# Optimization experiments

Hardware: AMD Instinct MI355X
Metric: run time of the kernel (lower is better)

## Reference

```python
import jax, jax.numpy as jnp
import numpy as np


def _gelu(x):
    # torch nn.GELU default is the exact erf form
    return jax.nn.gelu(x, approximate=False)


def setup_inputs() -> dict:
    key = jax.random.key(0)
    B, C, H, W = 4, 64, 256, 256   # batch, width, grid
    L, M1, M2 = 2, 32, 32          # retained blocks, Fourier modes per corner
    HM, P, O = 128, 256, 1         # channel-MLP hidden, projection hidden, out channels
    ks = jax.random.split(key, 16)
    n = lambda k, s, sc=1.0: jax.random.normal(k, s, dtype=jnp.float32) * sc
    spec = 1.0 / (C * C)           # classic FNO spectral-weight init scale
    fan = 1.0 / np.sqrt(C).astype(np.float32)
    return {
        "x": n(ks[0], (B, C, H, W)),
        # spectral weights: last dim 2 = (real, imag); sw1 -> low-freq corner, sw2 -> high-freq corner
        "sw1": n(ks[1], (L, C, C, M1, M2, 2), spec),
        "sw2": n(ks[2], (L, C, C, M1, M2, 2), spec),
        "skip_w": n(ks[3], (L, C, C), fan),
        "skip_b": n(ks[4], (L, C), 0.01),
        "mlp_w1": n(ks[5], (L, HM, C), fan),
        "mlp_b1": n(ks[6], (L, HM), 0.01),
        "mlp_w2": n(ks[7], (L, C, HM), 1.0 / np.sqrt(HM).astype(np.float32)),
        "mlp_b2": n(ks[8], (L, C), 0.01),
        "mlp_skip_w": n(ks[9], (L, C, C), fan),
        "mlp_skip_b": n(ks[10], (L, C), 0.01),
        "proj_w1": n(ks[11], (P, C), fan),
        "proj_b1": n(ks[12], (P,), 0.01),
        "proj_w2": n(ks[13], (O, P), 1.0 / np.sqrt(P).astype(np.float32)),
        "proj_b2": n(ks[14], (O,), 0.01),
    }


def _chan(w, x, b):
    # 1x1 conv over channels: w [O,I], x [B,I,H,W], b [O]
    return jnp.einsum('oi,bihw->bohw', w, x) + b[None, :, None, None]


def reference(x, sw1, sw2, skip_w, skip_b, mlp_w1, mlp_b1, mlp_w2, mlp_b2,
              mlp_skip_w, mlp_skip_b, proj_w1, proj_b1, proj_w2, proj_b2):
    L, M1, M2 = sw1.shape[0], sw1.shape[3], sw1.shape[4]
    B, C, H, W = x.shape
    for l in range(L):
        # --- spectral convolution ---
        xft = jnp.fft.rfft2(x, axes=(-2, -1))            # [B,C,H,W//2+1] complex64
        w1 = sw1[l, ..., 0] + 1j * sw1[l, ..., 1]        # [C,C,M1,M2]
        w2 = sw2[l, ..., 0] + 1j * sw2[l, ..., 1]
        top = jnp.einsum('bixy,ioxy->boxy', xft[:, :, :M1, :M2], w1)
        bot = jnp.einsum('bixy,ioxy->boxy', xft[:, :, H - M1:, :M2], w2)
        oft = jnp.zeros(xft.shape, xft.dtype)
        oft = oft.at[:, :, :M1, :M2].set(top).at[:, :, H - M1:, :M2].set(bot)
        y = jnp.fft.irfft2(oft, s=(H, W), axes=(-2, -1))
        # --- pointwise skip + GELU ---
        x = _gelu(y + _chan(skip_w[l], x, skip_b[l]))
        # --- channel MLP (fc1 -> gelu -> fc2) with 1x1 skip + GELU ---
        h = _gelu(_chan(mlp_w1[l], x, mlp_b1[l]))
        y2 = _chan(mlp_w2[l], h, mlp_b2[l]) + _chan(mlp_skip_w[l], x, mlp_skip_b[l])
        x = _gelu(y2)
    # --- projection: fc1 -> gelu -> fc2 ---
    h = _gelu(_chan(proj_w1, x, proj_b1))
    return _chan(proj_w2, h, proj_b2)
```

## Files before the change

### kernel.cpp

```cpp
#include <hip/hip_runtime.h>
#include <math.h>


#define OFF_XA   0
#define OFF_XB   16777216
#define OFF_Z1   33554432
#define OFF_XF   37748736
#define OFF_OF   38797312
#define OFF_TBF  39845888
#define OFF_EH   39854080
#define OFF_EL   39862272
#define OFF_AFH  39870464
#define OFF_AFL  39903232
#define OFF_AIH  39936000
#define OFF_AIL  39968768
#define OFF_WBF  40001536


typedef __attribute__((ext_vector_type(8))) short short8b;
typedef __attribute__((ext_vector_type(4))) float f32x4;

__device__ __forceinline__ float gelu_f(float v) {
    float nu = v * fmaf(v * v, -0.10294345f, -2.3022078f);
    float e;
    asm("v_exp_f32 %0, %1" : "=v"(e) : "v"(nu));
    return v * __builtin_amdgcn_rcpf(1.0f + e);
}

__device__ __forceinline__ unsigned f2bf(float f) {
    unsigned int u = __float_as_uint(f);
    u += 0x7FFFu + ((u >> 16) & 1u);
    return u >> 16;
}

__device__ __forceinline__ unsigned cvtpk(float a, float b) {
    unsigned r;
    asm("v_cvt_pk_bf16_f32 %0, %1, %2" : "=v"(r) : "v"(a), "v"(b));
    return r;
}

__device__ __forceinline__ void gload_lds16(const void* g, void* l) {
    __builtin_amdgcn_global_load_lds(
        (const __attribute__((address_space(1))) unsigned int*)g,
        (__attribute__((address_space(3))) unsigned int*)l, 16, 0, 0);
}

__device__ __forceinline__ short8b ld_frag_i4(const unsigned short* base, int ch0, int px) {
    const uint2* p0 = (const uint2*)(base + (size_t)(ch0 >> 2) * 262144 + px * 4);
    const uint2* p1 = (const uint2*)(base + (size_t)((ch0 >> 2) + 1) * 262144 + px * 4);
    uint2 lo = *p0, hi = *p1;
    uint4 pk = {lo.x, lo.y, hi.x, hi.y};
    return *(short8b*)&pk;
}

__global__ __launch_bounds__(256) void init_tw(float* ws) {
    int idx = blockIdx.x * 256 + threadIdx.x;
    unsigned short* tbf = (unsigned short*)(ws + OFF_TBF);
    unsigned short* eh  = (unsigned short*)(ws + OFF_EH);
    unsigned short* el  = (unsigned short*)(ws + OFF_EL);
    unsigned short* afh = (unsigned short*)(ws + OFF_AFH);
    unsigned short* afl = (unsigned short*)(ws + OFF_AFL);
    unsigned short* aih = (unsigned short*)(ws + OFF_AIH);
    unsigned short* ail = (unsigned short*)(ws + OFF_AIL);
    const double PI128 = 3.14159265358979323846 / 128.0;
    if (idx < 16384) {
        int w = idx >> 6, k = idx & 63;
        int kx = k >> 1;
        int m = (kx * w) & 255;
        double a = (double)m * PI128;
        float sc = (kx == 0) ? (1.0f / 65536.0f) : (2.0f / 65536.0f);
        float v = (k & 1) ? (float)(-sin(a)) * sc : (float)cos(a) * sc;
        tbf[idx] = (unsigned short)f2bf(v);
    }
    int i2 = idx - 16384;
    if (i2 >= 0 && i2 < 16384) {
        int n = i2 >> 8, w = i2 & 255;
        int kx = n >> 1;
        int m = (kx * w) & 255;
        double a = (double)m * PI128;
        float v = (n & 1) ? (float)(-sin(a)) : (float)cos(a);
        unsigned h = f2bf(v);
        eh[i2] = (unsigned short)h;
        el[i2] = (unsigned short)f2bf(v - __uint_as_float(h << 16));
    }
    int i3 = idx - 32768;
    if (i3 >= 0 && i3 < 65536) {
        int n = i3 >> 9, k = i3 & 511;
        int j = n & 63, c = n >> 6;
        int h = k >> 1, d = k & 1;
        int ky = (j < 32) ? j : (192 + j);
        int m = (ky * h) & 255;
        double a = (double)m * PI128;
        float cv = (float)cos(a), sv = (float)sin(a);
        float v = (c == 0) ? (d ? sv : cv) : (d ? cv : -sv);
        unsigned hh = f2bf(v);
        afh[i3] = (unsigned short)hh;
        afl[i3] = (unsigned short)f2bf(v - __uint_as_float(hh << 16));
    }
    int i4 = idx - 98304;
    if (i4 >= 0 && i4 < 65536) {
        int c = i4 >> 15, rem = i4 & 32767;
        int h = rem >> 7, k = rem & 127;
        int j = k >> 1, d = k & 1;
        int ky = (j < 32) ? j : (192 + j);
        int m = (ky * h) & 255;
        double a = (double)m * PI128;
        float cv = (float)cos(a), sv = (float)sin(a);
        float v = (c == 0) ? (d ? -sv : cv) : (d ? cv : sv);
        unsigned hh = f2bf(v);
        aih[i4] = (unsigned short)hh;
        ail[i4] = (unsigned short)f2bf(v - __uint_as_float(hh << 16));
    }
}

__global__ __launch_bounds__(256) void k_cvt(const float* __restrict__ w1,
                                             const float* __restrict__ w2,
                                             const float* __restrict__ wsk,
                                             const float* __restrict__ pw1,
                                             const float* __restrict__ ssk,
                                             unsigned short* __restrict__ wb) {
    int idx = blockIdx.x * 256 + threadIdx.x;
    if (idx < 16384)       wb[idx] = (unsigned short)f2bf(w1[idx]);
    else if (idx < 32768)  wb[idx] = (unsigned short)f2bf(w2[idx - 16384]);
    else if (idx < 40960)  wb[idx] = (unsigned short)f2bf(wsk[idx - 32768]);
    else if (idx < 57344)  wb[idx] = (unsigned short)f2bf(pw1[idx - 40960]);
    else if (idx < 65536)  wb[idx] = (unsigned short)f2bf(ssk[idx - 57344]);
}

__global__ __launch_bounds__(256) void k_fwd_w_f32(const float* __restrict__ x,
                                                   float* __restrict__ X1f,
                                                   const unsigned short* __restrict__ EH,
                                                   const unsigned short* __restrict__ EL) {
    __shared__ __align__(16) unsigned short smEH[16384];
    __shared__ __align__(16) unsigned short smEL[16384];
    int t = threadIdx.x;
#pragma unroll
    for (int pass = 0; pass < 8; ++pass) {
        int g = pass * 256 + t;
        int rown = g >> 5, oct = g & 31;
        int dst = rown * 256 + ((oct ^ (rown & 7)) * 8);
        *(uint4*)&smEH[dst] = *(const uint4*)&EH[g * 8];
        *(uint4*)&smEL[dst] = *(const uint4*)&EL[g * 8];
    }
    __syncthreads();

    int lane = t & 63, wv = t >> 6;
    int col = lane & 15, grp = lane >> 4;
    size_t row0 = (size_t)blockIdx.x * 64;
    int row = wv * 16 + col;
    const float* rp = x + (row0 + row) * 256 + grp * 8;

    short8b bH[8], bL[8];
#pragma unroll
    for (int kb = 0; kb < 8; ++kb) {
        float4 v0 = *(const float4*)(rp + kb * 32);
        float4 v1 = *(const float4*)(rp + kb * 32 + 4);
        float vv[8] = {v0.x, v0.y, v0.z, v0.w, v1.x, v1.y, v1.z, v1.w};
        short8b vH, vL;
#pragma unroll
        for (int i = 0; i < 8; ++i) {
            unsigned h = f2bf(vv[i]);
            vH[i] = (short)h;
            vL[i] = (short)f2bf(vv[i] - __uint_as_float(h << 16));
        }
        bH[kb] = vH; bL[kb] = vL;
    }
#pragma unroll
    for (int ot = 0; ot < 4; ++ot) {
        int n = ot * 16 + col;
        const unsigned short* eh = &smEH[n * 256];
        const unsigned short* el = &smEL[n * 256];
        f32x4 acc = {0.f, 0.f, 0.f, 0.f};
#pragma unroll
        for (int kb = 0; kb < 8; ++kb) {
            int off = ((kb * 4 + grp) ^ (n & 7)) * 8;
            const short8b aH = *(const short8b*)&eh[off];
            const short8b aL = *(const short8b*)&el[off];
            acc = __builtin_amdgcn_mfma_f32_16x16x32_bf16(aH, bH[kb], acc, 0, 0, 0);
            acc = __builtin_amdgcn_mfma_f32_16x16x32_bf16(aH, bL[kb], acc, 0, 0, 0);
            acc = __builtin_amdgcn_mfma_f32_16x16x32_bf16(aL, bH[kb], acc, 0, 0, 0);
        }
        *(float4*)&X1f[(row0 + row) * 64 + ot * 16 + grp * 4] = *(float4*)&acc;
    }
}

__global__ __launch_bounds__(256) void k_fwd_w_bf16(const unsigned short* __restrict__ xb,
                                                    float* __restrict__ X1f,
                                                    const unsigned short* __restrict__ EH,
                                                    const unsigned short* __restrict__ EL) {
    __shared__ __align__(16) unsigned short smEH[16384];
    __shared__ __align__(16) unsigned short smEL[16384];
    int t = threadIdx.x;
#pragma unroll
    for (int pass = 0; pass < 8; ++pass) {
        int g = pass * 256 + t;
        int rown = g >> 5, oct = g & 31;
        int dst = rown * 256 + ((oct ^ (rown & 7)) * 8);
        *(uint4*)&smEH[dst] = *(const uint4*)&EH[g * 8];
        *(uint4*)&smEL[dst] = *(const uint4*)&EL[g * 8];
    }
    __syncthreads();

    int lane = t & 63, wv = t >> 6;
    int col = lane & 15, grp = lane >> 4;
    size_t row0 = (size_t)blockIdx.x * 64;
    int row = wv * 16 + col;
    const unsigned short* rp = xb + (row0 + row) * 256 + grp * 8;

    short8b bH[8];
#pragma unroll
    for (int kb = 0; kb < 8; ++kb)
        bH[kb] = *(const short8b*)(rp + kb * 32);
#pragma unroll
    for (int ot = 0; ot < 4; ++ot) {
        int n = ot * 16 + col;
        const unsigned short* eh = &smEH[n * 256];
        const unsigned short* el = &smEL[n * 256];
        f32x4 acc = {0.f, 0.f, 0.f, 0.f};
#pragma unroll
        for (int kb = 0; kb < 8; ++kb) {
            int off = ((kb * 4 + grp) ^ (n & 7)) * 8;
            const short8b aH = *(const short8b*)&eh[off];
            const short8b aL = *(const short8b*)&el[off];
            acc = __builtin_amdgcn_mfma_f32_16x16x32_bf16(aH, bH[kb], acc, 0, 0, 0);
            acc = __builtin_amdgcn_mfma_f32_16x16x32_bf16(aL, bH[kb], acc, 0, 0, 0);
        }
        *(float4*)&X1f[(row0 + row) * 64 + ot * 16 + grp * 4] = *(float4*)&acc;
    }
}

__global__ __launch_bounds__(256) void k_fwd_h(const float* __restrict__ X1f,
                                               float* __restrict__ XFre,
                                               float* __restrict__ XFim,
                                               const unsigned short* __restrict__ AFH,
                                               const unsigned short* __restrict__ AFL) {
    __shared__ __align__(16) unsigned short smH[32 * 512];
    int t = threadIdx.x;
    int plane = blockIdx.x;
    const float* xp = X1f + (size_t)plane * 16384;
#pragma unroll
    for (int pass = 0; pass < 16; ++pass) {
        int idx = pass * 256 + t;
        int h = idx >> 4, seg = idx & 15;
        float4 v = *(const float4*)(xp + h * 64 + seg * 4);
        int kx0 = seg * 2, kx1 = seg * 2 + 1;
        int k0 = 2 * h;
        int oct = k0 >> 3, e = k0 & 7;
        int b0 = oct ^ (kx0 & 7), b1 = oct ^ (kx1 & 7);
        *(unsigned*)&smH[kx0 * 512 + b0 * 8 + e] = cvtpk(v.x, v.y);
        *(unsigned*)&smH[kx1 * 512 + b1 * 8 + e] = cvtpk(v.z, v.w);
    }
    __syncthreads();
    int lane = t & 63, wv = t >> 6;
    int col = lane & 15, grp = lane >> 4;
#pragma unroll
    for (int mi = 0; mi < 2; ++mi) {
        int mt = wv * 2 + mi;
        const unsigned short* Ah = AFH + (mt * 16 + col) * 512;
        const unsigned short* Al = AFL + (mt * 16 + col) * 512;
        f32x4 acc0 = {0.f, 0.f, 0.f, 0.f}, acc1 = {0.f, 0.f, 0.f, 0.f};
#pragma unroll
        for (int kb = 0; kb < 16; ++kb) {
            short8b aH = *(const short8b*)&Ah[kb * 32 + grp * 8];
            short8b aL = *(const short8b*)&Al[kb * 32 + grp * 8];
#pragma unroll
            for (int nt = 0; nt < 2; ++nt) {
                int kx = nt * 16 + col;
                int blk = (kb * 4 + grp) ^ (kx & 7);
                short8b bH = *(const short8b*)&smH[kx * 512 + blk * 8];
                f32x4 a = (nt == 0) ? acc0 : acc1;
                a = __builtin_amdgcn_mfma_f32_16x16x32_bf16(aH, bH, a, 0, 0, 0);
                a = __builtin_amdgcn_mfma_f32_16x16x32_bf16(aL, bH, a, 0, 0, 0);
                if (nt == 0) acc0 = a; else acc1 = a;
            }
        }
#pragma unroll
        for (int nt = 0; nt < 2; ++nt) {
            int kx = nt * 16 + col;
            f32x4 a = (nt == 0) ? acc0 : acc1;
#pragma unroll
            for (int r = 0; r < 4; ++r) {
                int n = mt * 16 + grp * 4 + r;
                float* dst = (n < 64)
                    ? (XFre + (size_t)plane * 2048 + n * 32 + kx)
                    : (XFim + (size_t)plane * 2048 + (n - 64) * 32 + kx);
                *dst = a[r];
            }
        }
    }
}

__global__ __launch_bounds__(512) void k_modemul(const float* __restrict__ XFre,
                                                 const float* __restrict__ XFim,
                                                 const float2* __restrict__ sw1,
                                                 const float2* __restrict__ sw2,
                                                 float* __restrict__ OFT0,
                                                 float* __restrict__ OFT1, int l) {
    __shared__ __align__(16) unsigned char smBuf[2][36864];
    int t = threadIdx.x;
    int wv = t >> 6;
    int o0 = blockIdx.x * 32;
    int j  = blockIdx.y;
    int ih = blockIdx.z;
    int jj = (j < 32) ? j : (j - 32);
    const char* Wbase = (const char*)((j < 32) ? sw1 : sw2) + (size_t)l * 33554432
                      + (size_t)jj * 256;
    const char* XRb = (const char*)XFre + (size_t)j * 128;
    const char* XIb = (const char*)XFim + (size_t)j * 128;
    int ib0 = ih * 32;

    auto STAGE = [&](int c, int buf) {
        unsigned char* L = &smBuf[buf][0];
#pragma unroll
        for (int k = 0; k < 4; ++k) {
            int g = k * 512 + t;
            int gi = g >> 9, go = (g >> 4) & 31, gs = g & 15;
            const char* src = Wbase + (size_t)(ib0 + c * 4 + gi) * 524288
                            + (size_t)(o0 + go) * 8192 + gs * 16;
            gload_lds16(src, L + g * 16);
        }
        if (t < 256) {
            int d = t >> 7, b = (t >> 5) & 3, gi = (t >> 3) & 3, kq = t & 7;
            const char* xb = d ? XIb : XRb;
            const char* src = xb + (size_t)(b * 64 + ib0 + c * 4 + gi) * 8192 + kq * 16;
            gload_lds16(src, L + 32768 + t * 16);
        }
    };

    int oh = t >> 5, kx = t & 31;
    float ar[2][4], ai[2][4];
#pragma unroll
    for (int oo = 0; oo < 2; ++oo)
#pragma unroll
        for (int b = 0; b < 4; ++b) { ar[oo][b] = 0.f; ai[oo][b] = 0.f; }

    STAGE(0, 0);
    for (int c = 0; c < 8; ++c) {
        if (c + 1 < 8) {
            STAGE(c + 1, (c + 1) & 1);
            if (wv < 4) asm volatile("s_waitcnt vmcnt(5)" ::: "memory");
            else        asm volatile("s_waitcnt vmcnt(4)" ::: "memory");
        } else {
            asm volatile("s_waitcnt vmcnt(0)" ::: "memory");
        }
        __builtin_amdgcn_sched_barrier(0);
        __builtin_amdgcn_s_barrier();

        const unsigned char* L = &smBuf[c & 1][0];
#pragma unroll
        for (int i = 0; i < 4; ++i) {
            float2 w0 = *(const float2*)(L + (i * 32 + oh * 2) * 256 + kx * 8);
            float2 w1 = *(const float2*)(L + (i * 32 + oh * 2 + 1) * 256 + kx * 8);
            float xr[4], xi[4];
#pragma unroll
            for (int b = 0; b < 4; ++b) {
                xr[b] = *(const float*)(L + 32768 + ((b * 4 + i) * 128) + kx * 4);
                xi[b] = *(const float*)(L + 32768 + 2048 + ((b * 4 + i) * 128) + kx * 4);
            }
#pragma unroll
            for (int b = 0; b < 4; ++b) {
                ar[0][b] += xr[b] * w0.x - xi[b] * w0.y;
                ai[0][b] += xr[b] * w0.y + xi[b] * w0.x;
                ar[1][b] += xr[b] * w1.x - xi[b] * w1.y;
                ai[1][b] += xr[b] * w1.y + xi[b] * w1.x;
            }
        }
        asm volatile("s_waitcnt lgkmcnt(0)" ::: "memory");
        __builtin_amdgcn_sched_barrier(0);
        __builtin_amdgcn_s_barrier();
    }

    float* OP = (ih == 0) ? OFT0 : OFT1;
#pragma unroll
    for (int oo = 0; oo < 2; ++oo)
#pragma unroll
        for (int b = 0; b < 4; ++b) {
            float* d = OP + (size_t)(b * 64 + o0 + oh * 2 + oo) * 4096 + kx * 128 + 2 * j;
            d[0] = ar[oo][b];
            d[1] = ai[oo][b];
        }
}

__global__ __launch_bounds__(256) void k_inv_h(const float* __restrict__ OFT,
                                               const float* __restrict__ OFT2,
                                               float* __restrict__ Zre,
                                               float* __restrict__ Zim,
                                               const unsigned short* __restrict__ AIH,
                                               const unsigned short* __restrict__ AIL) {
    __shared__ __align__(16) unsigned short smH[32 * 128];
    int t = threadIdx.x;
    int plane = blockIdx.x;
    const float* op  = OFT  + (size_t)plane * 4096;
    const float* op2 = OFT2 + (size_t)plane * 4096;
#pragma unroll
    for (int pass = 0; pass < 4; ++pass) {
        int idx = pass * 256 + t;
        int kx = idx >> 5, seg = idx & 31;
        float4 v  = *(const float4*)(op  + kx * 128 + seg * 4);
        float4 v2 = *(const float4*)(op2 + kx * 128 + seg * 4);
        v.x += v2.x; v.y += v2.y; v.z += v2.z; v.w += v2.w;
        int k0 = seg * 4;
        int oct = k0 >> 3, e = k0 & 7;
        int blk = oct ^ (kx & 7);
        uint2 ph = {cvtpk(v.x, v.y), cvtpk(v.z, v.w)};
        *(uint2*)&smH[kx * 128 + blk * 8 + e] = ph;
    }
    __syncthreads();
    int lane = t & 63, wv = t >> 6;
    int col = lane & 15, grp = lane >> 4;
#pragma unroll
    for (int mi = 0; mi < 4; ++mi) {
        int mt = wv * 4 + mi;
#pragma unroll
        for (int cc = 0; cc < 2; ++cc) {
            const unsigned short* Ah = AIH + cc * 32768 + (mt * 16 + col) * 128;
            const unsigned short* Al = AIL + cc * 32768 + (mt * 16 + col) * 128;
            f32x4 acc0 = {0.f, 0.f, 0.f, 0.f}, acc1 = {0.f, 0.f, 0.f, 0.f};
#pragma unroll
            for (int kb = 0; kb < 4; ++kb) {
                short8b aH = *(const short8b*)&Ah[kb * 32 + grp * 8];
                short8b aL = *(const short8b*)&Al[kb * 32 + grp * 8];
#pragma unroll
                for (int nt = 0; nt < 2; ++nt) {
                    int kx = nt * 16 + col;
                    int blk = (kb * 4 + grp) ^ (kx & 7);
                    short8b bH = *(const short8b*)&smH[kx * 128 + blk * 8];
                    f32x4 a = (nt == 0) ? acc0 : acc1;
                    a = __builtin_amdgcn_mfma_f32_16x16x32_bf16(aH, bH, a, 0, 0, 0);
                    a = __builtin_amdgcn_mfma_f32_16x16x32_bf16(aL, bH, a, 0, 0, 0);
                    if (nt == 0) acc0 = a; else acc1 = a;
                }
            }
            float* Zc = (cc == 0) ? Zre : Zim;
#pragma unroll
            for (int nt = 0; nt < 2; ++nt) {
                int kx = nt * 16 + col;
                f32x4 a = (nt == 0) ? acc0 : acc1;
#pragma unroll
                for (int r = 0; r < 4; ++r) {
                    int h = mt * 16 + grp * 4 + r;
                    Zc[(size_t)plane * 8192 + h * 32 + kx] = a[r];
                }
            }
        }
    }
}

template<int BF16IN>
__global__ __launch_bounds__(512) void k_invw_skip(const float* __restrict__ Zre,
                                                   const float* __restrict__ Zim,
                                                   const float* __restrict__ xinf,
                                                   const unsigned short* __restrict__ xinb,
                                                   const unsigned short* __restrict__ tbf,
                                                   const unsigned short* __restrict__ wsk,
                                                   const float* __restrict__ skip_b,
                                                   unsigned short* __restrict__ xout, int l) {
    __shared__ __align__(16) unsigned short smZ[64 * 64];
    int t = threadIdx.x;
    int hh = blockIdx.x, b = blockIdx.y;

    {
        int o = t >> 3, seg = t & 7;
        const float* zr = Zre + (size_t)(b * 64 + o) * 8192 + hh * 32 + seg * 4;
        const float* zi = Zim + (size_t)(b * 64 + o) * 8192 + hh * 32 + seg * 4;
        float4 r = *(const float4*)zr;
        float4 i = *(const float4*)zi;
        uint4 pk;
        pk.x = cvtpk(r.x, i.x);
        pk.y = cvtpk(r.y, i.y);
        pk.z = cvtpk(r.z, i.z);
        pk.w = cvtpk(r.w, i.w);
        int blk = seg ^ (o & 7);
        *(uint4*)&smZ[o * 64 + blk * 8] = pk;
    }

    int lane = t & 63, wv = t >> 6;
    int col = lane & 15, grp = lane >> 4;
    int w0 = wv * 32;

    short8b tf[2][2], bxf[2][2];
#pragma unroll
    for (int wt = 0; wt < 2; ++wt) {
        int w = w0 + wt * 16 + col;
#pragma unroll
        for (int kb = 0; kb < 2; ++kb) {
            tf[wt][kb] = *(const short8b*)&tbf[w * 64 + kb * 32 + grp * 8];
            int ch0 = kb * 32 + grp * 8;
            short8b v;
            if (BF16IN) {
                const unsigned short* xp = xinb + (size_t)(b * 64 + ch0) * 65536 + hh * 256 + w;
#pragma unroll
                for (int i = 0; i < 8; ++i) v[i] = (short)xp[(size_t)i * 65536];
            } else {
                const float* xp = xinf + (size_t)(b * 64 + ch0) * 65536 + hh * 256 + w;
#pragma unroll
                for (int i = 0; i < 8; ++i) v[i] = (short)f2bf(xp[(size_t)i * 65536]);
            }
            bxf[wt][kb] = v;
        }
    }
    __syncthreads();

    unsigned short* xo = xout + (size_t)b * 4194304;
    const unsigned short* WSp = wsk + l * 4096;
#pragma unroll
    for (int ot = 0; ot < 4; ++ot) {
        int o = ot * 16 + col;
        short8b az[2], ask[2];
#pragma unroll
        for (int kb = 0; kb < 2; ++kb) {
            int blk = (kb * 4 + grp) ^ (o & 7);
            az[kb] = *(const short8b*)&smZ[o * 64 + blk * 8];
            ask[kb] = *(const short8b*)&WSp[o * 64 + kb * 32 + grp * 8];
        }
        f32x4 bias = *(const f32x4*)&skip_b[l * 64 + ot * 16 + grp * 4];
#pragma unroll
        for (int wt = 0; wt < 2; ++wt) {
            f32x4 acc = bias;
            acc = __builtin_amdgcn_mfma_f32_16x16x32_bf16(az[0], tf[wt][0], acc, 0, 0, 0);
            acc = __builtin_amdgcn_mfma_f32_16x16x32_bf16(az[1], tf[wt][1], acc, 0, 0, 0);
            acc = __builtin_amdgcn_mfma_f32_16x16x32_bf16(ask[0], bxf[wt][0], acc, 0, 0, 0);
            acc = __builtin_amdgcn_mfma_f32_16x16x32_bf16(ask[1], bxf[wt][1], acc, 0, 0, 0);
            uint2 pk;
            pk.x = cvtpk(gelu_f(acc[0]), gelu_f(acc[1]));
            pk.y = cvtpk(gelu_f(acc[2]), gelu_f(acc[3]));
            int obase = ot * 16 + grp * 4;
            int px = hh * 256 + w0 + wt * 16 + col;
            *(uint2*)&xo[(size_t)(obase >> 2) * 262144 + px * 4] = pk;
        }
    }
}

template<int OUT4>
__global__ __launch_bounds__(512) void k_mlp(const unsigned short* __restrict__ xin,
                                             const unsigned short* __restrict__ wb,
                                             const float* __restrict__ b1,
                                             const float* __restrict__ b2,
                                             const float* __restrict__ bsk,
                                             unsigned short* __restrict__ xout, int l) {
    __shared__ __align__(16) unsigned short smemH[128 * 128];
    __shared__ __align__(16) unsigned short smW1[8192];
    __shared__ __align__(16) unsigned short smW2[8192];
    __shared__ __align__(16) unsigned short smWS[4096];
    int t = threadIdx.x;
    int b = blockIdx.y;
    int p0 = blockIdx.x * 128;

    const unsigned short* W1p = wb + l * 8192;
    const unsigned short* W2p = wb + 16384 + l * 8192;
    const unsigned short* WSp = wb + 32768 + l * 4096;
#pragma unroll
    for (int pass = 0; pass < 2; ++pass) {
        int g = pass * 512 + t;
        int row = g >> 3, oct = g & 7;
        *(uint4*)&smW1[row * 64 + ((oct ^ (row & 7)) * 8)] = *(const uint4*)&W1p[g * 8];
    }
#pragma unroll
    for (int pass = 0; pass < 2; ++pass) {
        int g = pass * 512 + t;
        int row = g >> 4, oct = g & 15;
        *(uint4*)&smW2[row * 128 + ((oct ^ (row & 7)) * 8)] = *(const uint4*)&W2p[g * 8];
    }
    if (t < 512) {
        int g = t;
        int row = g >> 3, oct = g & 7;
        *(uint4*)&smWS[row * 64 + ((oct ^ (row & 7)) * 8)] = *(const uint4*)&WSp[g * 8];
    }

    int lane = t & 63, wv = t >> 6;
    int col = lane & 15, grp = lane >> 4;
    int pxl = wv * 16 + col;
    int px = p0 + pxl;

    const unsigned short* xi = xin + (size_t)b * 4194304;
    short8b bx[2];
#pragma unroll
    for (int kb = 0; kb < 2; ++kb)
        bx[kb] = ld_frag_i4(xi, kb * 32 + grp * 8, px);
    __syncthreads();

#pragma unroll
    for (int ot = 0; ot < 8; ++ot) {
        int n1 = ot * 16 + col;
        short8b a0 = *(const short8b*)&smW1[n1 * 64 + ((grp ^ (n1 & 7)) * 8)];
        short8b a1 = *(const short8b*)&smW1[n1 * 64 + (((4 + grp) ^ (n1 & 7)) * 8)];
        int hm0 = ot * 16 + grp * 4;
        f32x4 acc = *(const f32x4*)&b1[l * 128 + hm0];
        acc = __builtin_amdgcn_mfma_f32_16x16x32_bf16(a0, bx[0], acc, 0, 0, 0);
        acc = __builtin_amdgcn_mfma_f32_16x16x32_bf16(a1, bx[1], acc, 0, 0, 0);
        uint2 hp;
        hp.x = cvtpk(gelu_f(acc[0]), gelu_f(acc[1]));
        hp.y = cvtpk(gelu_f(acc[2]), gelu_f(acc[3]));
        int blk = (hm0 >> 3) ^ (pxl & 7);
        *(uint2*)&smemH[pxl * 128 + blk * 8 + (hm0 & 7)] = hp;
    }

    short8b bh[4];
#pragma unroll
    for (int kb = 0; kb < 4; ++kb) {
        int blk = (kb * 4 + grp) ^ (pxl & 7);
        bh[kb] = *(const short8b*)&smemH[pxl * 128 + blk * 8];
    }

#pragma unroll
    for (int ot = 0; ot < 4; ++ot) {
        int o0 = ot * 16 + grp * 4;
        int n2 = ot * 16 + col;
        f32x4 acc = *(const f32x4*)&b2[l * 64 + o0];
        acc += *(const f32x4*)&bsk[l * 64 + o0];
        short8b a2[4], as[2];
#pragma unroll
        for (int kb = 0; kb < 4; ++kb)
            a2[kb] = *(const short8b*)&smW2[n2 * 128 + (((kb * 4 + grp) ^ (n2 & 7)) * 8)];
#pragma unroll
        for (int kb = 0; kb < 2; ++kb)
            as[kb] = *(const short8b*)&smWS[n2 * 64 + (((kb * 4 + grp) ^ (n2 & 7)) * 8)];
#pragma unroll
        for (int kb = 0; kb < 4; ++kb)
            acc = __builtin_amdgcn_mfma_f32_16x16x32_bf16(a2[kb], bh[kb], acc, 0, 0, 0);
#pragma unroll
        for (int kb = 0; kb < 2; ++kb)
            acc = __builtin_amdgcn_mfma_f32_16x16x32_bf16(as[kb], bx[kb], acc, 0, 0, 0);
        uint2 pk;
        pk.x = cvtpk(gelu_f(acc[0]), gelu_f(acc[1]));
        pk.y = cvtpk(gelu_f(acc[2]), gelu_f(acc[3]));
        if (OUT4) {
            unsigned short* xo = xout + (size_t)b * 4194304;
            *(uint2*)&xo[(size_t)(o0 >> 2) * 262144 + px * 4] = pk;
        } else {
            unsigned short* op = xout + (size_t)(b * 64 + o0) * 65536 + px;
            op[0]         = (unsigned short)(pk.x & 0xFFFF);
            op[65536]     = (unsigned short)(pk.x >> 16);
            op[2 * 65536] = (unsigned short)(pk.y & 0xFFFF);
            op[3 * 65536] = (unsigned short)(pk.y >> 16);
        }
    }
}

__global__ __launch_bounds__(512) void k_proj(const unsigned short* __restrict__ xin,
                                              const unsigned short* __restrict__ wb,
                                              const float* __restrict__ pb1,
                                              const float* __restrict__ pw2,
                                              const float* __restrict__ pb2,
                                              float* __restrict__ out) {
    __shared__ __align__(16) unsigned short smP1[16384];
    int t = threadIdx.x;
    int b = blockIdx.y;
    int p0 = blockIdx.x * 128;

    const unsigned short* P1p = wb + 40960;
#pragma unroll
    for (int pass = 0; pass < 4; ++pass) {
        int g = pass * 512 + t;
        int row = g >> 3, oct = g & 7;
        *(uint4*)&smP1[row * 64 + ((oct ^ (row & 7)) * 8)] = *(const uint4*)&P1p[g * 8];
    }

    int lane = t & 63, wv = t >> 6;
    int col = lane & 15, grp = lane >> 4;
    int px = p0 + wv * 16 + col;

    const unsigned short* xi = xin + (size_t)b * 4194304;
    short8b bx[2];
#pragma unroll
    for (int kb = 0; kb < 2; ++kb)
        bx[kb] = ld_frag_i4(xi, kb * 32 + grp * 8, px);
    __syncthreads();

    float psum = 0.f;
#pragma unroll
    for (int ot = 0; ot < 16; ++ot) {
        int n = ot * 16 + col;
        short8b a0 = *(const short8b*)&smP1[n * 64 + ((grp ^ (n & 7)) * 8)];
        short8b a1 = *(const short8b*)&smP1[n * 64 + (((4 + grp) ^ (n & 7)) * 8)];
        int o0 = ot * 16 + grp * 4;
        f32x4 b1v = *(const f32x4*)&pb1[o0];
        f32x4 w2v = *(const f32x4*)&pw2[o0];
        f32x4 acc = b1v;
        acc = __builtin_amdgcn_mfma_f32_16x16x32_bf16(a0, bx[0], acc, 0, 0, 0);
        acc = __builtin_amdgcn_mfma_f32_16x16x32_bf16(a1, bx[1], acc, 0, 0, 0);
        psum += w2v[0] * gelu_f(acc[0]) + w2v[1] * gelu_f(acc[1])
              + w2v[2] * gelu_f(acc[2]) + w2v[3] * gelu_f(acc[3]);
    }
    psum += __shfl_xor(psum, 16);
    psum += __shfl_xor(psum, 32);
    if (grp == 0)
        out[(size_t)b * 65536 + px] = psum + pb2[0];
}

extern "C" void kernel_launch(void* const* d_in, const int* in_sizes, int n_in,
                              void* d_out, int out_size, void* d_ws, size_t ws_size,
                              hipStream_t stream) {
    const float* x          = (const float*)d_in[0];
    const float2* sw1       = (const float2*)d_in[1];
    const float2* sw2       = (const float2*)d_in[2];
    const float* skip_w     = (const float*)d_in[3];
    const float* skip_b     = (const float*)d_in[4];
    const float* mlp_w1     = (const float*)d_in[5];
    const float* mlp_b1     = (const float*)d_in[6];
    const float* mlp_w2     = (const float*)d_in[7];
    const float* mlp_b2     = (const float*)d_in[8];
    const float* mlp_skip_w = (const float*)d_in[9];
    const float* mlp_skip_b = (const float*)d_in[10];
    const float* proj_w1    = (const float*)d_in[11];
    const float* proj_b1    = (const float*)d_in[12];
    const float* proj_w2    = (const float*)d_in[13];
    const float* proj_b2    = (const float*)d_in[14];

    float* ws = (float*)d_ws;
    unsigned short* XA4  = (unsigned short*)(ws + OFF_XA);
    unsigned short* XBb  = (unsigned short*)(ws + OFF_XB);
    unsigned short* XB4  = (unsigned short*)(ws + OFF_XB) + 16777216;
    float* X1f = ws + OFF_Z1;
    float* Zre = ws + OFF_Z1;
    float* Zim = ws + OFF_Z1 + 2097152;
    float* XFre = ws + OFF_XF;
    float* XFim = ws + OFF_XF + 524288;
    float* OFT = ws + OFF_OF;
    float* OFT2 = ws + OFF_XA;
    const unsigned short* TBF = (const unsigned short*)(ws + OFF_TBF);
    const unsigned short* EH  = (const unsigned short*)(ws + OFF_EH);
    const unsigned short* EL  = (const unsigned short*)(ws + OFF_EL);
    const unsigned short* AFH = (const unsigned short*)(ws + OFF_AFH);
    const unsigned short* AFL = (const unsigned short*)(ws + OFF_AFL);
    const unsigned short* AIH = (const unsigned short*)(ws + OFF_AIH);
    const unsigned short* AIL = (const unsigned short*)(ws + OFF_AIL);
    unsigned short* WB = (unsigned short*)(ws + OFF_WBF);

    init_tw<<<640, 256, 0, stream>>>(ws);
    k_cvt<<<256, 256, 0, stream>>>(mlp_w1, mlp_w2, mlp_skip_w, proj_w1, skip_w, WB);

    k_fwd_w_f32<<<1024, 256, 0, stream>>>(x, X1f, EH, EL);
    k_fwd_h<<<256, 256, 0, stream>>>(X1f, XFre, XFim, AFH, AFL);
    k_modemul<<<dim3(2, 64, 2), 512, 0, stream>>>(XFre, XFim, sw1, sw2, OFT, OFT2, 0);
    k_inv_h<<<256, 256, 0, stream>>>(OFT, OFT2, Zre, Zim, AIH, AIL);
    k_invw_skip<0><<<dim3(256, 4), 512, 0, stream>>>(Zre, Zim, x, nullptr, TBF,
                                                     WB + 57344, skip_b, XA4, 0);
    k_mlp<0><<<dim3(512, 4), 512, 0, stream>>>(XA4, WB, mlp_b1, mlp_b2, mlp_skip_b, XBb, 0);

    k_fwd_w_bf16<<<1024, 256, 0, stream>>>(XBb, X1f, EH, EL);
    k_fwd_h<<<256, 256, 0, stream>>>(X1f, XFre, XFim, AFH, AFL);
    k_modemul<<<dim3(2, 64, 2), 512, 0, stream>>>(XFre, XFim, sw1, sw2, OFT, OFT2, 1);
    k_inv_h<<<256, 256, 0, stream>>>(OFT, OFT2, Zre, Zim, AIH, AIL);
    k_invw_skip<1><<<dim3(256, 4), 512, 0, stream>>>(Zre, Zim, nullptr, XBb, TBF,
                                                     WB + 57344, skip_b, XA4, 1);
    k_mlp<1><<<dim3(512, 4), 512, 0, stream>>>(XA4, WB, mlp_b1, mlp_b2, mlp_skip_b, XB4, 1);

    k_proj<<<dim3(512, 4), 512, 0, stream>>>(XB4, WB, proj_b1, proj_w2, proj_b2,
                                             (float*)d_out);
}
```

Before: 286.3 us.

## Repartition spectral mode-multiply by output-channel pairs with four-way input-channel split

The mode-multiply kernel is restructured so each block covers two output channels, one quarter of the input channels and one corner, with each thread owning two contiguous modes. Weight staging becomes fully contiguous 16 KB slabs per input channel, and the spectral inputs are read straight from global memory instead of being staged in LDS. Partial sums from the four input-channel groups go to a partial buffer, and the inverse-H kernel now reduces those four partials instead of two. The aim is coalesced weight streaming and a simpler output layout, at the cost of more partial-sum traffic and uncached global reads of the activations.

Measured after the change: 363.2 us. 26.9% more time.

```diff
diff --git a/kernel.cpp b/kernel.cpp
--- a/kernel.cpp
+++ b/kernel.cpp
@@ -180,7 +180,7 @@
             acc = __builtin_amdgcn_mfma_f32_16x16x32_bf16(aH, bL[kb], acc, 0, 0, 0);
             acc = __builtin_amdgcn_mfma_f32_16x16x32_bf16(aL, bH[kb], acc, 0, 0, 0);
         }
-        *(float4*)&X1f[(row0 + row) * 64 + ot * 16 + grp * 4] = *(float4*)&acc;
+        *(f32x4*)&X1f[(row0 + row) * 64 + ot * 16 + grp * 4] = acc;
     }
 }
 
@@ -225,7 +225,7 @@
             acc = __builtin_amdgcn_mfma_f32_16x16x32_bf16(aH, bH[kb], acc, 0, 0, 0);
             acc = __builtin_amdgcn_mfma_f32_16x16x32_bf16(aL, bH[kb], acc, 0, 0, 0);
         }
-        *(float4*)&X1f[(row0 + row) * 64 + ot * 16 + grp * 4] = *(float4*)&acc;
+        *(f32x4*)&X1f[(row0 + row) * 64 + ot * 16 + grp * 4] = acc;
     }
 }
 
@@ -294,52 +294,52 @@
                                                  const float* __restrict__ XFim,
                                                  const float2* __restrict__ sw1,
                                                  const float2* __restrict__ sw2,
-                                                 float* __restrict__ OFT0,
-                                                 float* __restrict__ OFT1, int l) {
-    __shared__ __align__(16) unsigned char smBuf[2][36864];
+                                                 float* __restrict__ P, int l) {
+    __shared__ __align__(16) unsigned char smBuf[2][32768];
     int t = threadIdx.x;
-    int wv = t >> 6;
-    int o0 = blockIdx.x * 32;
-    int j  = blockIdx.y;
-    int ih = blockIdx.z;
-    int jj = (j < 32) ? j : (j - 32);
-    const char* Wbase = (const char*)((j < 32) ? sw1 : sw2) + (size_t)l * 33554432
-                      + (size_t)jj * 256;
-    const char* XRb = (const char*)XFre + (size_t)j * 128;
-    const char* XIb = (const char*)XFim + (size_t)j * 128;
-    int ib0 = ih * 32;
+    int o0 = blockIdx.x * 2;
+    int iq = blockIdx.y;
+    int tb = blockIdx.z;
+    const char* Wb = (const char*)(tb ? sw2 : sw1) + (size_t)l * 33554432
+                   + (size_t)o0 * 8192;
+    int i0 = iq * 16;
 
     auto STAGE = [&](int c, int buf) {
         unsigned char* L = &smBuf[buf][0];
 #pragma unroll
         for (int k = 0; k < 4; ++k) {
             int g = k * 512 + t;
-            int gi = g >> 9, go = (g >> 4) & 31, gs = g & 15;
-            const char* src = Wbase + (size_t)(ib0 + c * 4 + gi) * 524288
-                            + (size_t)(o0 + go) * 8192 + gs * 16;
+            const char* src = Wb + (size_t)(i0 + c * 2 + (g >> 10)) * 524288
+                            + (size_t)(g & 1023) * 16;
             gload_lds16(src, L + g * 16);
         }
-        if (t < 256) {
-            int d = t >> 7, b = (t >> 5) & 3, gi = (t >> 3) & 3, kq = t & 7;
-            const char* xb = d ? XIb : XRb;
-            const char* src = xb + (size_t)(b * 64 + ib0 + c * 4 + gi) * 8192 + kq * 16;
-            gload_lds16(src, L + 32768 + t * 16);
-        }
     };
 
-    int oh = t >> 5, kx = t & 31;
-    float ar[2][4], ai[2][4];
-#pragma unroll
-    for (int oo = 0; oo < 2; ++oo)
-#pragma unroll
-        for (int b = 0; b < 4; ++b) { ar[oo][b] = 0.f; ai[oo][b] = 0.f; }
+    int m0 = t * 2;
+    const float* Xr = XFre + tb * 1024 + m0;
+    const float* Xi = XFim + tb * 1024 + m0;
+
+    f32x4 acc[2][4];
+#pragma unroll
+    for (int o = 0; o < 2; ++o)
+#pragma unroll
+        for (int b = 0; b < 4; ++b) acc[o][b] = (f32x4){0.f, 0.f, 0.f, 0.f};
 
     STAGE(0, 0);
     for (int c = 0; c < 8; ++c) {
-        if (c + 1 < 8) {
+        float2 xr[2][4], xi[2][4];
+#pragma unroll
+        for (int iloc = 0; iloc < 2; ++iloc) {
+            int i = i0 + c * 2 + iloc;
+#pragma unroll
+            for (int b = 0; b < 4; ++b) {
+                xr[iloc][b] = *(const float2*)(Xr + (size_t)(b * 64 + i) * 2048);
+                xi[iloc][b] = *(const float2*)(Xi + (size_t)(b * 64 + i) * 2048);
+            }
+        }
+        if (c < 7) {
             STAGE(c + 1, (c + 1) & 1);
-            if (wv < 4) asm volatile("s_waitcnt vmcnt(5)" ::: "memory");
-            else        asm volatile("s_waitcnt vmcnt(4)" ::: "memory");
+            asm volatile("s_waitcnt vmcnt(4)" ::: "memory");
         } else {
             asm volatile("s_waitcnt vmcnt(0)" ::: "memory");
         }
@@ -348,21 +348,20 @@
 
         const unsigned char* L = &smBuf[c & 1][0];
 #pragma unroll
-        for (int i = 0; i < 4; ++i) {
-            float2 w0 = *(const float2*)(L + (i * 32 + oh * 2) * 256 + kx * 8);
-            float2 w1 = *(const float2*)(L + (i * 32 + oh * 2 + 1) * 256 + kx * 8);
-            float xr[4], xi[4];
+        for (int iloc = 0; iloc < 2; ++iloc) {
+            float4 w0 = *(const float4*)(L + iloc * 16384 + m0 * 8);
+            float4 w1 = *(const float4*)(L + iloc * 16384 + 8192 + m0 * 8);
 #pragma unroll
             for (int b = 0; b < 4; ++b) {
-                xr[b] = *(const float*)(L + 32768 + ((b * 4 + i) * 128) + kx * 4);
-                xi[b] = *(const float*)(L + 32768 + 2048 + ((b * 4 + i) * 128) + kx * 4);
-            }
-#pragma unroll
-            for (int b = 0; b < 4; ++b) {
-                ar[0][b] += xr[b] * w0.x - xi[b] * w0.y;
-                ai[0][b] += xr[b] * w0.y + xi[b] * w0.x;
-                ar[1][b] += xr[b] * w1.x - xi[b] * w1.y;
-                ai[1][b] += xr[b] * w1.y + xi[b] * w1.x;
+                float2 r = xr[iloc][b], im = xi[iloc][b];
+                acc[0][b].x += r.x * w0.x - im.x * w0.y;
+                acc[0][b].y += r.x * w0.y + im.x * w0.x;
+                acc[0][b].z += r.y * w0.z - im.y * w0.w;
+                acc[0][b].w += r.y * w0.w + im.y * w0.z;
+                acc[1][b].x += r.x * w1.x - im.x * w1.y;
+                acc[1][b].y += r.x * w1.y + im.x * w1.x;
+                acc[1][b].z += r.y * w1.z - im.y * w1.w;
+                acc[1][b].w += r.y * w1.w + im.y * w1.z;
             }
         }
         asm volatile("s_waitcnt lgkmcnt(0)" ::: "memory");
@@ -370,19 +369,17 @@
         __builtin_amdgcn_s_barrier();
     }
 
-    float* OP = (ih == 0) ? OFT0 : OFT1;
-#pragma unroll
-    for (int oo = 0; oo < 2; ++oo)
+    float* Pq = P + (size_t)iq * 1048576;
+#pragma unroll
+    for (int o = 0; o < 2; ++o)
 #pragma unroll
         for (int b = 0; b < 4; ++b) {
-            float* d = OP + (size_t)(b * 64 + o0 + oh * 2 + oo) * 4096 + kx * 128 + 2 * j;
-            d[0] = ar[oo][b];
-            d[1] = ai[oo][b];
-        }
-}
-
-__global__ __launch_bounds__(256) void k_inv_h(const float* __restrict__ OFT,
-                                               const float* __restrict__ OFT2,
+            float* d = Pq + (size_t)(b * 64 + o0 + o) * 4096 + (tb * 1024 + m0) * 2;
+            *(f32x4*)d = acc[o][b];
+        }
+}
+
+__global__ __launch_bounds__(256) void k_inv_h(const float* __restrict__ P,
                                                float* __restrict__ Zre,
                                                float* __restrict__ Zim,
                                                const unsigned short* __restrict__ AIH,
@@ -390,20 +387,30 @@
     __shared__ __align__(16) unsigned short smH[32 * 128];
     int t = threadIdx.x;
     int plane = blockIdx.x;
-    const float* op  = OFT  + (size_t)plane * 4096;
-    const float* op2 = OFT2 + (size_t)plane * 4096;
+    const float* p0 = P + (size_t)plane * 4096;
 #pragma unroll
     for (int pass = 0; pass < 4; ++pass) {
         int idx = pass * 256 + t;
-        int kx = idx >> 5, seg = idx & 31;
-        float4 v  = *(const float4*)(op  + kx * 128 + seg * 4);
-        float4 v2 = *(const float4*)(op2 + kx * 128 + seg * 4);
-        v.x += v2.x; v.y += v2.y; v.z += v2.z; v.w += v2.w;
-        int k0 = seg * 4;
-        int oct = k0 >> 3, e = k0 & 7;
-        int blk = oct ^ (kx & 7);
-        uint2 ph = {cvtpk(v.x, v.y), cvtpk(v.z, v.w)};
-        *(uint2*)&smH[kx * 128 + blk * 8 + e] = ph;
+        float4 v  = *(const float4*)(p0 + idx * 4);
+        float4 v1 = *(const float4*)(p0 + 1048576 + idx * 4);
+        float4 v2 = *(const float4*)(p0 + 2097152 + idx * 4);
+        float4 v3 = *(const float4*)(p0 + 3145728 + idx * 4);
+        v.x += v1.x + v2.x + v3.x;  v.y += v1.y + v2.y + v3.y;
+        v.z += v1.z + v2.z + v3.z;  v.w += v1.w + v2.w + v3.w;
+        int m = idx * 2;
+        {
+            int j = m >> 5, kx = m & 31;
+            int k0 = 2 * j, oct = k0 >> 3, e = k0 & 7;
+            int blk = oct ^ (kx & 7);
+            *(unsigned*)&smH[kx * 128 + blk * 8 + e] = cvtpk(v.x, v.y);
+        }
+        {
+            int m2 = m + 1;
+            int j = m2 >> 5, kx = m2 & 31;
+            int k0 = 2 * j, oct = k0 >> 3, e = k0 & 7;
+            int blk = oct ^ (kx & 7);
+            *(unsigned*)&smH[kx * 128 + blk * 8 + e] = cvtpk(v.z, v.w);
+        }
     }
     __syncthreads();
     int lane = t & 63, wv = t >> 6;
@@ -716,8 +723,7 @@
     float* Zim = ws + OFF_Z1 + 2097152;
     float* XFre = ws + OFF_XF;
     float* XFim = ws + OFF_XF + 524288;
-    float* OFT = ws + OFF_OF;
-    float* OFT2 = ws + OFF_XA;
+    float* Pp = ws + OFF_XA;
     const unsigned short* TBF = (const unsigned short*)(ws + OFF_TBF);
     const unsigned short* EH  = (const unsigned short*)(ws + OFF_EH);
     const unsigned short* EL  = (const unsigned short*)(ws + OFF_EL);
@@ -732,16 +738,16 @@
 
     k_fwd_w_f32<<<1024, 256, 0, stream>>>(x, X1f, EH, EL);
     k_fwd_h<<<256, 256, 0, stream>>>(X1f, XFre, XFim, AFH, AFL);
-    k_modemul<<<dim3(2, 64, 2), 512, 0, stream>>>(XFre, XFim, sw1, sw2, OFT, OFT2, 0);
-    k_inv_h<<<256, 256, 0, stream>>>(OFT, OFT2, Zre, Zim, AIH, AIL);
+    k_modemul<<<dim3(32, 4, 2), 512, 0, stream>>>(XFre, XFim, sw1, sw2, Pp, 0);
+    k_inv_h<<<256, 256, 0, stream>>>(Pp, Zre, Zim, AIH, AIL);
     k_invw_skip<0><<<dim3(256, 4), 512, 0, stream>>>(Zre, Zim, x, nullptr, TBF,
                                                      WB + 57344, skip_b, XA4, 0);
     k_mlp<0><<<dim3(512, 4), 512, 0, stream>>>(XA4, WB, mlp_b1, mlp_b2, mlp_skip_b, XBb, 0);
 
     k_fwd_w_bf16<<<1024, 256, 0, stream>>>(XBb, X1f, EH, EL);
     k_fwd_h<<<256, 256, 0, stream>>>(X1f, XFre, XFim, AFH, AFL);
-    k_modemul<<<dim3(2, 64, 2), 512, 0, stream>>>(XFre, XFim, sw1, sw2, OFT, OFT2, 1);
-    k_inv_h<<<256, 256, 0, stream>>>(OFT, OFT2, Zre, Zim, AIH, AIL);
+    k_modemul<<<dim3(32, 4, 2), 512, 0, stream>>>(XFre, XFim, sw1, sw2, Pp, 1);
+    k_inv_h<<<256, 256, 0, stream>>>(Pp, Zre, Zim, AIH, AIL);
     k_invw_skip<1><<<dim3(256, 4), 512, 0, stream>>>(Zre, Zim, nullptr, XBb, TBF,
                                                      WB + 57344, skip_b, XA4, 1);
     k_mlp<1><<<dim3(512, 4), 512, 0, stream>>>(XA4, WB, mlp_b1, mlp_b2, mlp_skip_b, XB4, 1);
```
